# Kernel optimization log

Hardware: AMD Instinct MI355X
Metric: run time of the kernel (lower is better)

Reference implementation:

```python
import jax, jax.numpy as jnp
import numpy as np

N_EMBEDS = 1024
N_HEADS = 16
EPS = 1e-3


def layer_norm(x, gamma, beta):
    mean = jnp.mean(x, axis=-1, keepdims=True)
    var = jnp.mean((x - mean) ** 2, axis=-1, keepdims=True)
    return gamma * (x - mean) / jnp.sqrt(var + EPS) + beta


def setup_inputs() -> dict:
    key = jax.random.key(0)
    ks = jax.random.split(key, 8)
    B, T, C = 4, 2048, N_EMBEDS
    s = 1.0 / np.sqrt(C)
    return {
        "x": jax.random.normal(ks[0], (B, T, C), dtype=jnp.float32),
        "w_qkv": jax.random.normal(ks[1], (C, 3 * C), dtype=jnp.float32) * s,
        "w_proj": jax.random.normal(ks[2], (C, C), dtype=jnp.float32) * s,
        "b_proj": jnp.zeros((C,), dtype=jnp.float32),
        "w1": jax.random.normal(ks[3], (C, 4 * C), dtype=jnp.float32) * s,
        "b1": jnp.zeros((4 * C,), dtype=jnp.float32),
        "w2": jax.random.normal(ks[4], (4 * C, C), dtype=jnp.float32) * (0.5 / np.sqrt(C)),
        "b2": jnp.zeros((C,), dtype=jnp.float32),
        "gamma1": jnp.ones((C,), dtype=jnp.float32),
        "beta1": jnp.zeros((C,), dtype=jnp.float32),
        "gamma2": jnp.ones((C,), dtype=jnp.float32),
        "beta2": jnp.zeros((C,), dtype=jnp.float32),
    }


def reference(x, w_qkv, w_proj, b_proj, w1, b1, w2, b2, gamma1, beta1, gamma2, beta2):
    B, T, C = x.shape
    H = N_HEADS
    D = C // H
    scale = D ** -0.5

    # --- attention sub-layer (pre-LN) ---
    h = layer_norm(x, gamma1, beta1)
    qkv = h @ w_qkv                      # [B,T,3C]
    q, k, v = jnp.split(qkv, 3, axis=-1)
    q = q.reshape(B, T, H, D).transpose(0, 2, 1, 3)  # [B,H,T,D]
    k = k.reshape(B, T, H, D).transpose(0, 2, 1, 3)
    v = v.reshape(B, T, H, D).transpose(0, 2, 1, 3)
    att = jnp.einsum('bhqd,bhkd->bhqk', q, k) * scale
    causal = jnp.tril(jnp.ones((T, T), dtype=bool))
    att = jnp.where(causal[None, None], att, jnp.float32(-1e9))
    att = jax.nn.softmax(att, axis=-1)
    out = jnp.einsum('bhqk,bhkd->bhqd', att, v)
    out = out.transpose(0, 2, 1, 3).reshape(B, T, C)
    x = x + out @ w_proj + b_proj

    # --- FFN sub-layer (pre-LN, erf-GELU) ---
    h = layer_norm(x, gamma2, beta2)
    h = jax.nn.gelu(h @ w1 + b1, approximate=False)
    x = x + h @ w2 + b2
    return x
```

## Files before the change

### kernel.cpp

```cpp
#include <hip/hip_runtime.h>
#include <hip/hip_bf16.h>
#include <cstdint>
#include <cstddef>

#define B_ 4
#define T_ 2048
#define C_ 1024
#define H_ 16
#define D_ 64
#define M_ (B_*T_)

using bf16_t = __hip_bfloat16;
typedef __bf16 v8bf __attribute__((ext_vector_type(8)));
typedef float  v4f  __attribute__((ext_vector_type(4)));
typedef float  f32x16 __attribute__((ext_vector_type(16)));

#define QSCALE (0.125f * 1.44269504088896340736f)

static __device__ __forceinline__ bf16_t f2bf(float v){ return __float2bfloat16(v); }
static __device__ __forceinline__ float bfraw2f(unsigned short u){
  union { unsigned int i; float f; } c; c.i = ((unsigned int)u) << 16; return c.f;
}

static __device__ __forceinline__ void glds16(const bf16_t* g, bf16_t* l){
  __builtin_amdgcn_global_load_lds((__attribute__((address_space(1))) void*)g,
                                   (__attribute__((address_space(3))) void*)l, 16, 0, 0);
}

static __device__ __forceinline__ uint32_t cvt_pk_bf16(float lo, float hi){
  uint32_t w;
  asm("v_cvt_pk_bf16_f32 %0, %1, %2" : "=v"(w) : "v"(lo), "v"(hi));
  return w;
}

static __device__ __forceinline__ float gelu_fast(float x){
  const float u = __builtin_fmaf(0.044715f * x * x, x, x);
  const float e = __builtin_amdgcn_exp2f(2.3021256637f * u);
  return x - x * __builtin_amdgcn_rcpf(1.0f + e);
}

__global__ void k_transpose_all(const float* __restrict__ in0, bf16_t* __restrict__ out0,
                                const float* __restrict__ in1, bf16_t* __restrict__ out1,
                                const float* __restrict__ in2, bf16_t* __restrict__ out2,
                                const float* __restrict__ in3, bf16_t* __restrict__ out3){
  __shared__ float tile[32][33];
  const int bid = blockIdx.x;
  const float* in; bf16_t* out; int K, N, lb;
  if (bid < 3072)      { in=in0; out=out0; K=1024; N=3072; lb=bid; }
  else if (bid < 4096) { in=in1; out=out1; K=1024; N=1024; lb=bid-3072; }
  else if (bid < 8192) { in=in2; out=out2; K=1024; N=4096; lb=bid-4096; }
  else                 { in=in3; out=out3; K=4096; N=1024; lb=bid-8192; }
  const int nbx = N >> 5;
  const int k0 = (lb / nbx) * 32, n0 = (lb % nbx) * 32;
  const int tx = threadIdx.x, ty = threadIdx.y;
  #pragma unroll
  for(int j=0;j<32;j+=8) tile[ty+j][tx] = in[(size_t)(k0+ty+j)*N + n0+tx];
  __syncthreads();
  #pragma unroll
  for(int j=0;j<32;j+=8) out[(size_t)(n0+ty+j)*K + k0+tx] = f2bf(tile[tx][ty+j]);
}

__global__ __launch_bounds__(256) void k_layernorm(const float* __restrict__ x,
                                                   const float* __restrict__ gamma,
                                                   const float* __restrict__ beta,
                                                   bf16_t* __restrict__ out){
  int row = blockIdx.x;
  int tid = threadIdx.x;
  const float4 v = reinterpret_cast<const float4*>(x + (size_t)row*C_)[tid];
  float s  = v.x+v.y+v.z+v.w;
  float ss = v.x*v.x+v.y*v.y+v.z*v.z+v.w*v.w;
  #pragma unroll
  for(int m=1;m<64;m<<=1){ s += __shfl_xor(s,m); ss += __shfl_xor(ss,m); }
  __shared__ float sbuf[4], ssbuf[4];
  int wid = tid>>6, lane = tid&63;
  if(lane==0){ sbuf[wid]=s; ssbuf[wid]=ss; }
  __syncthreads();
  s  = sbuf[0]+sbuf[1]+sbuf[2]+sbuf[3];
  ss = ssbuf[0]+ssbuf[1]+ssbuf[2]+ssbuf[3];
  float mean = s * (1.0f/C_);
  float var  = ss * (1.0f/C_) - mean*mean;
  float rstd = rsqrtf(var + 1e-3f);
  const float4 g = reinterpret_cast<const float4*>(gamma)[tid];
  const float4 b = reinterpret_cast<const float4*>(beta)[tid];
  union { ushort4 u; bf16_t h[4]; } pk;
  pk.h[0] = f2bf(g.x*(v.x-mean)*rstd + b.x);
  pk.h[1] = f2bf(g.y*(v.y-mean)*rstd + b.y);
  pk.h[2] = f2bf(g.z*(v.z-mean)*rstd + b.z);
  pk.h[3] = f2bf(g.w*(v.w-mean)*rstd + b.w);
  *reinterpret_cast<ushort4*>(out + (size_t)row*C_ + tid*4) = pk.u;
}

__global__ __launch_bounds__(256)
void k_add2(const bf16_t* __restrict__ p0, const bf16_t* __restrict__ p1,
            const float* __restrict__ bias, float* out){
  const int row = blockIdx.x, tid = threadIdx.x;
  float4 xr = reinterpret_cast<const float4*>(out + (size_t)row*C_)[tid];
  const ushort4 a = reinterpret_cast<const ushort4*>(p0 + (size_t)row*C_)[tid];
  const ushort4 b = reinterpret_cast<const ushort4*>(p1 + (size_t)row*C_)[tid];
  const float4 g = reinterpret_cast<const float4*>(bias)[tid];
  xr.x += bfraw2f(a.x) + bfraw2f(b.x) + g.x;
  xr.y += bfraw2f(a.y) + bfraw2f(b.y) + g.y;
  xr.z += bfraw2f(a.z) + bfraw2f(b.z) + g.z;
  xr.w += bfraw2f(a.w) + bfraw2f(b.w) + g.w;
  reinterpret_cast<float4*>(out + (size_t)row*C_)[tid] = xr;
}

template<int MODE>
__global__ __launch_bounds__(512, 1)
void k_gemm9(const bf16_t* __restrict__ A, const bf16_t* __restrict__ Bt,
             const float* __restrict__ bias, const float* resid,
             void* out0, void* out1, void* out2,
             int N, int ld, int klen, int gx, int tc)
{
  __shared__ __align__(16) bf16_t As[2][2][128*64];
  __shared__ __align__(16) bf16_t Bs[2][2][128*64];
  const int tid = threadIdx.x, lane = tid & 63, w = tid >> 6;
  const int wm = w >> 2, wn = w & 3;
  const int koff = blockIdx.z * klen;

  const int sswz = ((lane & 7) ^ ((lane >> 3) & 7)) * 8;
  const int srow = w * 8 + (lane >> 3);

  int row0, col0;
  const bf16_t *Agb, *Bgb;
  auto set_tile = [&](int tile){
    const int swz = (tile & 7) * (tc >> 3) + (tile >> 3);
    const int ct = swz % gx, rt = swz / gx;
    row0 = rt * 256; col0 = ct * 256;
    Agb = A  + (size_t)(row0 + srow) * ld + koff + sswz;
    Bgb = Bt + (size_t)(col0 + srow) * ld + koff + sswz;
  };

  auto stageA = [&](int tt, int hh){
    const bf16_t* src = Agb + (size_t)(hh * 128) * ld + tt * 64;
    bf16_t* dst = &As[tt & 1][hh][w * 512];
    glds16(src, dst);
    glds16(src + (size_t)64 * ld, dst + 4096);
  };
  auto stageB = [&](int tt, int hh){
    const bf16_t* src = Bgb + (size_t)(hh * 128) * ld + tt * 64;
    bf16_t* dst = &Bs[tt & 1][hh][w * 512];
    glds16(src, dst);
    glds16(src + (size_t)64 * ld, dst + 4096);
  };
  auto stage_prologue = [&](){
    stageA(0,0); stageA(0,1); stageB(0,0); stageB(0,1);
    stageB(1,0); stageB(1,1); stageA(1,0);
  };

  v8bf af[4][2], bfv[4][2];
  v4f acc[8][4];

  auto LDA = [&](int bb, int mh){
    const bf16_t* base = &As[bb][wm][0];
    #pragma unroll
    for (int m = 0; m < 4; ++m)
      #pragma unroll
      for (int kk = 0; kk < 2; ++kk) {
        const int r  = mh*64 + m*16 + (lane & 15);
        const int sl = (kk*4 + (lane >> 4)) ^ (lane & 7);
        af[m][kk] = *reinterpret_cast<const v8bf*>(base + r*64 + sl*8);
      }
  };
  auto LDB4 = [&](int bb, int nh){
    const bf16_t* base = &Bs[bb][wn >> 1][0];
    #pragma unroll
    for (int n = 0; n < 2; ++n)
      #pragma unroll
      for (int kk = 0; kk < 2; ++kk) {
        const int r  = (wn & 1)*64 + (nh*2+n)*16 + (lane & 15);
        const int sl = (kk*4 + (lane >> 4)) ^ (lane & 7);
        bfv[nh*2+n][kk] = *reinterpret_cast<const v8bf*>(base + r*64 + sl*8);
      }
  };

#define MFMA_Q(mh_, nh_) \
  __builtin_amdgcn_s_setprio(1); \
  _Pragma("unroll") \
  for (int kk = 0; kk < 2; ++kk) \
    _Pragma("unroll") \
    for (int m = 0; m < 4; ++m) \
      _Pragma("unroll") \
      for (int n = 0; n < 2; ++n) \
        acc[(mh_)*4+m][(nh_)*2+n] = __builtin_amdgcn_mfma_f32_16x16x32_bf16( \
            af[m][kk], bfv[(nh_)*2+n][kk], acc[(mh_)*4+m][(nh_)*2+n], 0,0,0); \
  __builtin_amdgcn_s_setprio(0);

#define BAR()   __builtin_amdgcn_s_barrier()
#define LGKM0() do { asm volatile("s_waitcnt lgkmcnt(0)" ::: "memory"); \
                     __builtin_amdgcn_sched_barrier(0); } while(0)

  const int NP = (klen >> 6) >> 1;
  int tile = blockIdx.x;
  set_tile(tile);
  stage_prologue();

  for (;;) {
    asm volatile("s_waitcnt vmcnt(6)" ::: "memory");
    BAR();
    #pragma unroll
    for (int mf = 0; mf < 8; ++mf)
      #pragma unroll
      for (int nf = 0; nf < 4; ++nf)
        acc[mf][nf] = (v4f){0.f, 0.f, 0.f, 0.f};

    for (int j = 0; j < NP; ++j) {
      const int t2 = 2*j + 2, t3 = 2*j + 3;
      const bool more = (j + 1 < NP);
      LDA(0, 0); LDB4(0, 0);
      stageA(2*j + 1, 1);
      BAR(); LGKM0(); MFMA_Q(0, 0); BAR();
      LDB4(0, 1);
      if (more) stageB(t2, 0);
      BAR(); LGKM0(); MFMA_Q(0, 1); BAR();
      LDA(0, 1);
      if (more) stageB(t2, 1);
      BAR(); LGKM0(); MFMA_Q(1, 0); BAR();
      if (more) { stageA(t2, 0); asm volatile("s_waitcnt vmcnt(6)" ::: "memory"); }
      else      {                asm volatile("s_waitcnt vmcnt(0)" ::: "memory"); }
      BAR(); MFMA_Q(1, 1); BAR();
      LDA(1, 0); LDB4(1, 0);
      if (more) stageA(t2, 1);
      BAR(); LGKM0(); MFMA_Q(0, 0); BAR();
      LDB4(1, 1);
      if (more) stageB(t3, 0);
      BAR(); LGKM0(); MFMA_Q(0, 1); BAR();
      LDA(1, 1);
      if (more) stageB(t3, 1);
      BAR(); LGKM0(); MFMA_Q(1, 0); BAR();
      if (more) { stageA(t3, 0); asm volatile("s_waitcnt vmcnt(6)" ::: "memory"); }
      else      {                asm volatile("s_waitcnt vmcnt(0)" ::: "memory"); }
      BAR(); MFMA_Q(1, 1); BAR();
    }

    const int erow0 = row0, ecol0 = col0;
    const int next = tile + (int)gridDim.x;
    const bool have_next = (next < tc);
    if (have_next) { set_tile(next); stage_prologue(); }

    #pragma unroll
    for (int mf = 0; mf < 8; ++mf) {
      const int rbase = erow0 + wm*128 + mf*16 + (lane>>4)*4;
      #pragma unroll
      for (int nf = 0; nf < 4; ++nf) {
        const int c = ecol0 + wn*64 + nf*16 + (lane&15);
        #pragma unroll
        for (int i = 0; i < 4; ++i) {
          const int rr = rbase + i;
          float v = acc[mf][nf][i];
          if constexpr(MODE==0){
            const int sec = c >> 10, cc = c & 1023;
            const int h = cc >> 6, d = cc & 63;
            const int b = rr >> 11, t = rr & 2047;
            if(sec==0)      ((bf16_t*)out0)[((size_t)(b*H_ + h)*T_ + t)*D_ + d] = f2bf(v * QSCALE);
            else if(sec==1) ((bf16_t*)out1)[((size_t)(b*H_ + h)*T_ + t)*D_ + d] = f2bf(v);
            else            ((bf16_t*)out2)[((size_t)(b*H_ + h)*D_ + d)*T_ + t] = f2bf(v);
          } else if constexpr(MODE==2){
            ((bf16_t*)out0)[(size_t)rr*N + c] = f2bf(gelu_fast(v + bias[c]));
          } else {
            bf16_t* dst = blockIdx.z ? (bf16_t*)out1 : (bf16_t*)out0;
            dst[(size_t)rr*N + c] = f2bf(v);
          }
        }
      }
    }
    if (!have_next) break;
    tile = next;
  }
#undef MFMA_Q
#undef BAR
#undef LGKM0
}

__global__ __launch_bounds__(512, 1)
void k_gemm8(const bf16_t* __restrict__ A, const bf16_t* __restrict__ Bt,
             const float* __restrict__ bias, const float* resid,
             float* out0, int N, int K, int gx)
{
  __shared__ __align__(16) bf16_t As[2][256*64];
  __shared__ __align__(16) bf16_t Bs[3][128*64];
  const int tid = threadIdx.x, lane = tid & 63, w = tid >> 6;
  const int wm = w >> 1, wn = w & 1;

  const int nwg = gx * 32;
  const int orig = blockIdx.y * gx + blockIdx.x;
  const int swz = (orig & 7) * (nwg >> 3) + (orig >> 3);
  const int ct = swz % gx, rt = swz / gx;
  const int row0 = rt * 256, col0 = ct * 128;

  const int sswz = ((lane & 7) ^ ((lane >> 3) & 7)) * 8;
  const int srow = w * 8 + (lane >> 3);
  const bf16_t* Agb = A  + (size_t)(row0 + srow) * K + sswz;
  const bf16_t* Bgb = Bt + (size_t)(col0 + srow) * K + sswz;

  auto stageA = [&](int tt){
    const bf16_t* src = Agb + tt * 64;
    bf16_t* dst = &As[tt & 1][w * 512];
    #pragma unroll
    for (int i = 0; i < 4; ++i)
      glds16(src + (size_t)(i*64) * K, dst + i*4096);
  };
  auto stageB = [&](int tt){
    const bf16_t* src = Bgb + tt * 64;
    bf16_t* dst = &Bs[tt % 3][w * 512];
    #pragma unroll
    for (int i = 0; i < 2; ++i)
      glds16(src + (size_t)(i*64) * K, dst + i*4096);
  };

  v8bf af[4][2], bfv[4][2];
  v4f acc[4][4] = {};

  auto LDA = [&](int ab){
    const bf16_t* base = &As[ab][0];
    #pragma unroll
    for (int m = 0; m < 4; ++m)
      #pragma unroll
      for (int kk = 0; kk < 2; ++kk) {
        const int r  = wm*64 + m*16 + (lane & 15);
        const int sl = (kk*4 + (lane >> 4)) ^ (lane & 7);
        af[m][kk] = *reinterpret_cast<const v8bf*>(base + r*64 + sl*8);
      }
  };
  auto LDB = [&](int bb, int nh){
    const bf16_t* base = &Bs[bb][0];
    #pragma unroll
    for (int n = 0; n < 2; ++n)
      #pragma unroll
      for (int kk = 0; kk < 2; ++kk) {
        const int r  = wn*64 + (nh*2+n)*16 + (lane & 15);
        const int sl = (kk*4 + (lane >> 4)) ^ (lane & 7);
        bfv[nh*2+n][kk] = *reinterpret_cast<const v8bf*>(base + r*64 + sl*8);
      }
  };

#define MFMA_Q(nh_) \
  __builtin_amdgcn_s_setprio(1); \
  _Pragma("unroll") \
  for (int kk = 0; kk < 2; ++kk) \
    _Pragma("unroll") \
    for (int m = 0; m < 4; ++m) \
      _Pragma("unroll") \
      for (int n = 0; n < 2; ++n) \
        acc[m][(nh_)*2+n] = __builtin_amdgcn_mfma_f32_16x16x32_bf16( \
            af[m][kk], bfv[(nh_)*2+n][kk], acc[m][(nh_)*2+n], 0,0,0); \
  __builtin_amdgcn_s_setprio(0);

#define BAR()   __builtin_amdgcn_s_barrier()
#define LGKM0() do { asm volatile("s_waitcnt lgkmcnt(0)" ::: "memory"); \
                     __builtin_amdgcn_sched_barrier(0); } while(0)
#define VM6()   asm volatile("s_waitcnt vmcnt(6)" ::: "memory")
#define VM0()   asm volatile("s_waitcnt vmcnt(0)" ::: "memory")

  const int NP = (K >> 6) >> 1;
  stageB(0); stageA(0); stageB(1); stageA(1);
  VM6();
  BAR();

  for (int j = 0; j < NP; ++j) {
    const int t0 = 2*j, t1 = 2*j + 1, t2 = 2*j + 2, t3 = 2*j + 3;
    const bool more = (j + 1 < NP);
    LDA(0); LDB(t0 % 3, 0);
    if (more) stageB(t2);
    BAR(); LGKM0(); MFMA_Q(0); BAR();
    LDB(t0 % 3, 1);
    if (more) { stageA(t2); VM6(); } else { VM0(); }
    BAR(); LGKM0(); MFMA_Q(1); BAR();
    LDA(1); LDB(t1 % 3, 0);
    if (more) stageB(t3);
    BAR(); LGKM0(); MFMA_Q(0); BAR();
    LDB(t1 % 3, 1);
    if (more) { stageA(t3); VM6(); } else { VM0(); }
    BAR(); LGKM0(); MFMA_Q(1); BAR();
  }
#undef MFMA_Q
#undef BAR
#undef LGKM0
#undef VM6
#undef VM0

  #pragma unroll
  for (int mf = 0; mf < 4; ++mf) {
    const int rbase = row0 + wm*64 + mf*16 + (lane>>4)*4;
    #pragma unroll
    for (int nf = 0; nf < 4; ++nf) {
      const int c = col0 + wn*64 + nf*16 + (lane&15);
      #pragma unroll
      for (int i = 0; i < 4; ++i) {
        const int rr = rbase + i;
        out0[(size_t)rr*N + c] = acc[mf][nf][i] + bias[c] + resid[(size_t)rr*N + c];
      }
    }
  }
}

__global__ __launch_bounds__(256)
void k_attn(const bf16_t* __restrict__ Q, const bf16_t* __restrict__ Kg,
            const bf16_t* __restrict__ Vt, bf16_t* __restrict__ O)
{
  __shared__ __align__(16) bf16_t Ks [64][72];
  __shared__ __align__(16) bf16_t Vts[64][72];
  __shared__ __align__(16) bf16_t Os [128][72];
  const int bh = blockIdx.y;
  const int pair = blockIdx.x;
  const int tid = threadIdx.x, lane = tid & 63, w = tid >> 6;
  const int ql = lane & 31, hi = lane >> 5;
  const int srow = tid >> 2;
  const int scol = (tid & 3) * 16;
  const bf16_t* Kgp = Kg + ((size_t)bh*T_ + srow)*D_ + scol;
  const bf16_t* Vtp = Vt + ((size_t)bh*D_ + srow)*T_ + scol;
  const int b = bh >> 4, h = bh & 15;

  for(int half=0; half<2; ++half){
    const int qt = half ? pair : (15 - pair);
    const int qbase = qt*128 + w*32;
    const int q = qbase + ql;

    v8bf qf[4];
    {
      const bf16_t* Qb = Q + ((size_t)bh*T_ + q)*D_ + hi*8;
      #pragma unroll
      for(int ds=0; ds<4; ds++)
        qf[ds] = *reinterpret_cast<const v8bf*>(Qb + ds*16);
    }

    f32x16 accO[2] = {};
    float mrun = -1e30f, lrun = 0.0f;
    const int NT = (qt + 1) * 2;

    v8bf kr0 = *reinterpret_cast<const v8bf*>(Kgp);
    v8bf kr1 = *reinterpret_cast<const v8bf*>(Kgp + 8);
    v8bf vr0 = *reinterpret_cast<const v8bf*>(Vtp);
    v8bf vr1 = *reinterpret_cast<const v8bf*>(Vtp + 8);

    for(int t=0; t<NT; t++){
      const int kv0 = t*64;
      *reinterpret_cast<v8bf*>(&Ks [srow][scol  ]) = kr0;
      *reinterpret_cast<v8bf*>(&Ks [srow][scol+8]) = kr1;
      *reinterpret_cast<v8bf*>(&Vts[srow][scol  ]) = vr0;
      *reinterpret_cast<v8bf*>(&Vts[srow][scol+8]) = vr1;
      __syncthreads();
      if(t+1 < NT){
        const size_t kn = (size_t)(kv0 + 64);
        kr0 = *reinterpret_cast<const v8bf*>(Kgp + kn*D_);
        kr1 = *reinterpret_cast<const v8bf*>(Kgp + kn*D_ + 8);
        vr0 = *reinterpret_cast<const v8bf*>(Vtp + kn);
        vr1 = *reinterpret_cast<const v8bf*>(Vtp + kn + 8);
      }

      if(kv0 <= qbase + 31){
        f32x16 sT[2] = {};
        #pragma unroll
        for(int kvh=0; kvh<2; kvh++)
          #pragma unroll
          for(int ds=0; ds<4; ds++){
            v8bf kf = *reinterpret_cast<const v8bf*>(&Ks[kvh*32 + ql][ds*16 + hi*8]);
            sT[kvh] = __builtin_amdgcn_mfma_f32_32x32x16_bf16(kf, qf[ds], sT[kvh], 0,0,0);
          }

        if(kv0 + 63 > qbase){
          const int qrel = q - kv0 - hi*4;
          #pragma unroll
          for(int kvh=0; kvh<2; kvh++)
            #pragma unroll
            for(int r=0; r<16; r++){
              const int c = kvh*32 + (r&3) + 8*(r>>2);
              if(c > qrel) sT[kvh][r] = -1e30f;
            }
        }

        float pm = sT[0][0];
        #pragma unroll
        for(int r=1; r<16; r++) pm = fmaxf(pm, sT[0][r]);
        #pragma unroll
        for(int r=0; r<16; r++) pm = fmaxf(pm, sT[1][r]);
        pm = fmaxf(pm, __shfl_xor(pm, 32));

        if(__any(pm - mrun > 8.0f)){
          const float mnew = fmaxf(mrun, pm);
          const float corr = __builtin_amdgcn_exp2f(mrun - mnew);
          mrun = mnew;
          lrun *= corr;
          #pragma unroll
          for(int dh=0; dh<2; dh++)
            #pragma unroll
            for(int r=0; r<16; r++) accO[dh][r] *= corr;
        }

        float rs = 0.0f;
        #pragma unroll
        for(int kvh=0; kvh<2; kvh++)
          #pragma unroll
          for(int r=0; r<16; r++){
            float p = __builtin_amdgcn_exp2f(sT[kvh][r] - mrun);
            sT[kvh][r] = p;
            rs += p;
          }
        rs += __shfl_xor(rs, 32);
        lrun += rs;

        v8bf pfrag[4];
        #pragma unroll
        for(int s4=0; s4<4; s4++){
          const int kvh = s4>>1, bb = (s4&1)*8;
          uint32_t wa = cvt_pk_bf16(sT[kvh][bb+0], sT[kvh][bb+1]);
          uint32_t wb = cvt_pk_bf16(sT[kvh][bb+2], sT[kvh][bb+3]);
          uint32_t wc = cvt_pk_bf16(sT[kvh][bb+4], sT[kvh][bb+5]);
          uint32_t wd = cvt_pk_bf16(sT[kvh][bb+6], sT[kvh][bb+7]);
          uint32_t xwa = (uint32_t)__shfl_xor((int)wa, 32);
          uint32_t xwb = (uint32_t)__shfl_xor((int)wb, 32);
          uint32_t xwc = (uint32_t)__shfl_xor((int)wc, 32);
          uint32_t xwd = (uint32_t)__shfl_xor((int)wd, 32);
          union { uint32_t u[4]; v8bf v; } pk;
          pk.u[0] = hi ? xwc : wa;
          pk.u[1] = hi ? xwd : wb;
          pk.u[2] = hi ? wc  : xwa;
          pk.u[3] = hi ? wd  : xwb;
          pfrag[s4] = pk.v;
        }

        #pragma unroll
        for(int dh=0; dh<2; dh++)
          #pragma unroll
          for(int s4=0; s4<4; s4++){
            v8bf vf = *reinterpret_cast<const v8bf*>(&Vts[dh*32 + ql][s4*16 + hi*8]);
            accO[dh] = __builtin_amdgcn_mfma_f32_32x32x16_bf16(vf, pfrag[s4], accO[dh], 0,0,0);
          }
      }
      __syncthreads();
    }

    const float inv = 1.0f / lrun;
    #pragma unroll
    for(int dh=0; dh<2; dh++)
      #pragma unroll
      for(int rg=0; rg<4; rg++){
        uint32_t lo_ = cvt_pk_bf16(accO[dh][rg*4+0]*inv, accO[dh][rg*4+1]*inv);
        uint32_t hi_ = cvt_pk_bf16(accO[dh][rg*4+2]*inv, accO[dh][rg*4+3]*inv);
        uint2 w2; w2.x = lo_; w2.y = hi_;
        *reinterpret_cast<uint2*>(&Os[w*32 + ql][dh*32 + rg*8 + hi*4]) = w2;
      }
    __syncthreads();
    const int orow = tid >> 1, ocol = (tid & 1) * 32;
    bf16_t* Og = O + ((size_t)(b*T_ + qt*128 + orow))*C_ + h*64 + ocol;
    #pragma unroll
    for(int j=0;j<4;j++)
      *reinterpret_cast<v8bf*>(Og + j*8) = *reinterpret_cast<const v8bf*>(&Os[orow][ocol + j*8]);
    __syncthreads();
  }
}

extern "C" void kernel_launch(void* const* d_in, const int* in_sizes, int n_in,
                              void* d_out, int out_size, void* d_ws, size_t ws_size,
                              hipStream_t stream) {
  const float* x      = (const float*)d_in[0];
  const float* w_qkv  = (const float*)d_in[1];
  const float* w_proj = (const float*)d_in[2];
  const float* b_proj = (const float*)d_in[3];
  const float* w1     = (const float*)d_in[4];
  const float* b1     = (const float*)d_in[5];
  const float* w2     = (const float*)d_in[6];
  const float* b2     = (const float*)d_in[7];
  const float* gamma1 = (const float*)d_in[8];
  const float* beta1  = (const float*)d_in[9];
  const float* gamma2 = (const float*)d_in[10];
  const float* beta2  = (const float*)d_in[11];

  char* ws = (char*)d_ws;
  bf16_t* wqkv_t  = (bf16_t*)(ws + 0);
  bf16_t* wproj_t = (bf16_t*)(ws + 6291456);
  bf16_t* w1_t    = (bf16_t*)(ws + 8388608);
  bf16_t* w2_t    = (bf16_t*)(ws + 16777216);
  bf16_t* qb      = (bf16_t*)(ws + 25165824);
  bf16_t* kb      = (bf16_t*)(ws + 41943040);
  bf16_t* vtb     = (bf16_t*)(ws + 58720256);
  bf16_t* obuf    = (bf16_t*)(ws + 75497472);
  bf16_t* hb      = (bf16_t*)(ws + 92274688);
  bf16_t* gb      = (bf16_t*)(ws + 25165824);
  float*  x2      = (float*)d_out;

  k_transpose_all<<<12288, dim3(32,8), 0, stream>>>(w_qkv, wqkv_t, w_proj, wproj_t,
                                                    w1, w1_t, w2, w2_t);

  k_layernorm<<<M_, 256, 0, stream>>>(x, gamma1, beta1, hb);

  k_gemm9<0><<<dim3(256, 1, 1), 512, 0, stream>>>(hb, wqkv_t, nullptr, nullptr,
                                                  qb, kb, vtb, 3072, 1024, 1024, 12, 384);
  k_attn<<<dim3(8, B_*H_), 256, 0, stream>>>(qb, kb, vtb, obuf);

  k_gemm8<<<dim3(8, 32), 512, 0, stream>>>(obuf, wproj_t, b_proj, x,
                                           x2, 1024, 1024, 8);
  k_layernorm<<<M_, 256, 0, stream>>>(x2, gamma2, beta2, hb);

  k_gemm9<2><<<dim3(256, 1, 1), 512, 0, stream>>>(hb, w1_t, b1, nullptr,
                                                  gb, nullptr, nullptr, 4096, 1024, 1024, 16, 512);
  k_gemm9<4><<<dim3(128, 1, 2), 512, 0, stream>>>(gb, w2_t, nullptr, nullptr,
                                                  obuf, hb, nullptr, 1024, 4096, 2048, 4, 128);
  k_add2<<<M_, 256, 0, stream>>>(obuf, hb, b2, x2);
}
```

Before: 369.4 us.

## Add 128x128-tile persistent GEMM kernel with 2 blocks/CU for FFN up-projection

Introduces k_gemmH, a persistent bf16 MFMA GEMM using 128x128 output tiles, 256-thread blocks and a two-stage K-pipelined LDS schedule with launch bounds allowing two workgroups per CU. It replaces the larger-tile 512-thread k_gemm9<2> for the FFN first matmul with GELU epilogue. The intent is better occupancy and latency hiding through smaller tiles and more concurrent workgroups. The cost is lower per-tile data reuse and more global traffic for A and B.

```diff
diff --git a/kernel.cpp b/kernel.cpp
--- a/kernel.cpp
+++ b/kernel.cpp
@@ -272,6 +272,157 @@
 #undef LGKM0
 }
 
+__global__ __launch_bounds__(256, 2)
+void k_gemmH(const bf16_t* __restrict__ A, const bf16_t* __restrict__ Bt,
+             const float* __restrict__ bias, bf16_t* __restrict__ out0,
+             int N, int ld, int klen, int gx, int tc)
+{
+  __shared__ __align__(16) bf16_t As[2][2][64*64];
+  __shared__ __align__(16) bf16_t Bs[2][2][64*64];
+  const int tid = threadIdx.x, lane = tid & 63, w = tid >> 6;
+  const int wm = w >> 1, wn = w & 1;
+
+  const int sswz = ((lane & 7) ^ ((lane >> 3) & 7)) * 8;
+  const int srow = w * 8 + (lane >> 3);
+
+  int row0, col0;
+  const bf16_t *Agb, *Bgb;
+  auto set_tile = [&](int tile){
+    const int swz = (tile & 7) * (tc >> 3) + (tile >> 3);
+    const int ct = swz % gx, rt = swz / gx;
+    row0 = rt * 128; col0 = ct * 128;
+    Agb = A  + (size_t)(row0 + srow) * ld + sswz;
+    Bgb = Bt + (size_t)(col0 + srow) * ld + sswz;
+  };
+
+  auto stageA = [&](int tt, int hh){
+    const bf16_t* src = Agb + (size_t)(hh * 64) * ld + tt * 64;
+    bf16_t* dst0 = &As[tt & 1][hh][w * 512];
+    glds16(src, dst0);
+    glds16(src + (size_t)32 * ld, dst0 + 2048);
+  };
+  auto stageB = [&](int tt, int hh){
+    const bf16_t* src = Bgb + (size_t)(hh * 64) * ld + tt * 64;
+    bf16_t* dst0 = &Bs[tt & 1][hh][w * 512];
+    glds16(src, dst0);
+    glds16(src + (size_t)32 * ld, dst0 + 2048);
+  };
+  auto stage_prologue = [&](){
+    stageA(0,0); stageA(0,1); stageB(0,0); stageB(0,1);
+    stageB(1,0); stageB(1,1); stageA(1,0);
+  };
+
+  v8bf af[2][2], bfv[4][2];
+  v4f acc[4][4];
+
+  auto LDA = [&](int bb, int mh){
+    const bf16_t* base = &As[bb][wm][0];
+    #pragma unroll
+    for (int m = 0; m < 2; ++m)
+      #pragma unroll
+      for (int kk = 0; kk < 2; ++kk) {
+        const int r  = mh*32 + m*16 + (lane & 15);
+        const int sl = (kk*4 + (lane >> 4)) ^ (lane & 7);
+        af[m][kk] = *reinterpret_cast<const v8bf*>(base + r*64 + sl*8);
+      }
+  };
+  auto LDB4 = [&](int bb, int nh){
+    const bf16_t* base = &Bs[bb][wn][0];
+    #pragma unroll
+    for (int n = 0; n < 2; ++n)
+      #pragma unroll
+      for (int kk = 0; kk < 2; ++kk) {
+        const int r  = (nh*2+n)*16 + (lane & 15);
+        const int sl = (kk*4 + (lane >> 4)) ^ (lane & 7);
+        bfv[nh*2+n][kk] = *reinterpret_cast<const v8bf*>(base + r*64 + sl*8);
+      }
+  };
+
+#define MFMA_Q(mh_, nh_) \
+  __builtin_amdgcn_s_setprio(1); \
+  _Pragma("unroll") \
+  for (int kk = 0; kk < 2; ++kk) \
+    _Pragma("unroll") \
+    for (int m = 0; m < 2; ++m) \
+      _Pragma("unroll") \
+      for (int n = 0; n < 2; ++n) \
+        acc[(mh_)*2+m][(nh_)*2+n] = __builtin_amdgcn_mfma_f32_16x16x32_bf16( \
+            af[m][kk], bfv[(nh_)*2+n][kk], acc[(mh_)*2+m][(nh_)*2+n], 0,0,0); \
+  __builtin_amdgcn_s_setprio(0);
+
+#define BAR()   __builtin_amdgcn_s_barrier()
+#define LGKM0() do { asm volatile("s_waitcnt lgkmcnt(0)" ::: "memory"); \
+                     __builtin_amdgcn_sched_barrier(0); } while(0)
+
+  const int NP = (klen >> 6) >> 1;
+  int tile = blockIdx.x;
+  set_tile(tile);
+  stage_prologue();
+
+  for (;;) {
+    asm volatile("s_waitcnt vmcnt(6)" ::: "memory");
+    BAR();
+    #pragma unroll
+    for (int mf = 0; mf < 4; ++mf)
+      #pragma unroll
+      for (int nf = 0; nf < 4; ++nf)
+        acc[mf][nf] = (v4f){0.f, 0.f, 0.f, 0.f};
+
+    for (int j = 0; j < NP; ++j) {
+      const int t2 = 2*j + 2, t3 = 2*j + 3;
+      const bool more = (j + 1 < NP);
+      LDA(0, 0); LDB4(0, 0);
+      stageA(2*j + 1, 1);
+      BAR(); LGKM0(); MFMA_Q(0, 0); BAR();
+      LDB4(0, 1);
+      if (more) stageB(t2, 0);
+      BAR(); LGKM0(); MFMA_Q(0, 1); BAR();
+      LDA(0, 1);
+      if (more) stageB(t2, 1);
+      BAR(); LGKM0(); MFMA_Q(1, 0); BAR();
+      if (more) { stageA(t2, 0); asm volatile("s_waitcnt vmcnt(6)" ::: "memory"); }
+      else      {                asm volatile("s_waitcnt vmcnt(0)" ::: "memory"); }
+      BAR(); MFMA_Q(1, 1); BAR();
+      LDA(1, 0); LDB4(1, 0);
+      if (more) stageA(t2, 1);
+      BAR(); LGKM0(); MFMA_Q(0, 0); BAR();
+      LDB4(1, 1);
+      if (more) stageB(t3, 0);
+      BAR(); LGKM0(); MFMA_Q(0, 1); BAR();
+      LDA(1, 1);
+      if (more) stageB(t3, 1);
+      BAR(); LGKM0(); MFMA_Q(1, 0); BAR();
+      if (more) { stageA(t3, 0); asm volatile("s_waitcnt vmcnt(6)" ::: "memory"); }
+      else      {                asm volatile("s_waitcnt vmcnt(0)" ::: "memory"); }
+      BAR(); MFMA_Q(1, 1); BAR();
+    }
+
+    const int erow0 = row0, ecol0 = col0;
+    const int next = tile + (int)gridDim.x;
+    const bool have_next = (next < tc);
+    if (have_next) { set_tile(next); stage_prologue(); }
+
+    #pragma unroll
+    for (int mf = 0; mf < 4; ++mf) {
+      const int rbase = erow0 + wm*64 + mf*16 + (lane>>4)*4;
+      #pragma unroll
+      for (int nf = 0; nf < 4; ++nf) {
+        const int c = ecol0 + wn*64 + nf*16 + (lane&15);
+        #pragma unroll
+        for (int i = 0; i < 4; ++i) {
+          const int rr = rbase + i;
+          out0[(size_t)rr*N + c] = f2bf(gelu_fast(acc[mf][nf][i] + bias[c]));
+        }
+      }
+    }
+    if (!have_next) break;
+    tile = next;
+  }
+#undef MFMA_Q
+#undef BAR
+#undef LGKM0
+}
+
 __global__ __launch_bounds__(512, 1)
 void k_gemm8(const bf16_t* __restrict__ A, const bf16_t* __restrict__ Bt,
              const float* __restrict__ bias, const float* resid,
@@ -592,8 +743,8 @@
                                            x2, 1024, 1024, 8);
   k_layernorm<<<M_, 256, 0, stream>>>(x2, gamma2, beta2, hb);
 
-  k_gemm9<2><<<dim3(256, 1, 1), 512, 0, stream>>>(hb, w1_t, b1, nullptr,
-                                                  gb, nullptr, nullptr, 4096, 1024, 1024, 16, 512);
+  k_gemmH<<<dim3(512, 1, 1), 256, 0, stream>>>(hb, w1_t, b1, gb,
+                                               4096, 1024, 1024, 32, 2048);
   k_gemm9<4><<<dim3(128, 1, 2), 512, 0, stream>>>(gb, w2_t, nullptr, nullptr,
                                                   obuf, hb, nullptr, 1024, 4096, 2048, 4, 128);
   k_add2<<<M_, 256, 0, stream>>>(obuf, hb, b2, x2);
```

Result: slower. 380.4 us (+3.0%).

## Restructure GEMM main loop into two half-phases with full A-fragment loads

Applied to the files above, without the earlier changes.

Loads all eight A fragments per K-tile at once and runs 8x2 MFMA blocks per phase, so each K-tile takes two barrier-delimited phases instead of four. The B and A global-to-LDS stage issues are regrouped to match. This halves the number of barriers and LDS wait points per K-tile, aiming to cut synchronization overhead. In exchange it holds twice as many A-fragment registers, which raises VGPR pressure, and it bunches the global loads into fewer, larger bursts.

```diff
diff --git a/kernel.cpp b/kernel.cpp
--- a/kernel.cpp
+++ b/kernel.cpp
@@ -148,19 +148,21 @@
     stageB(1,0); stageB(1,1); stageA(1,0);
   };
 
-  v8bf af[4][2], bfv[4][2];
+  v8bf af[8][2], bfv[4][2];
   v4f acc[8][4];
 
-  auto LDA = [&](int bb, int mh){
+  auto LDA16 = [&](int bb){
     const bf16_t* base = &As[bb][wm][0];
     #pragma unroll
-    for (int m = 0; m < 4; ++m)
-      #pragma unroll
-      for (int kk = 0; kk < 2; ++kk) {
-        const int r  = mh*64 + m*16 + (lane & 15);
-        const int sl = (kk*4 + (lane >> 4)) ^ (lane & 7);
-        af[m][kk] = *reinterpret_cast<const v8bf*>(base + r*64 + sl*8);
-      }
+    for (int mh = 0; mh < 2; ++mh)
+      #pragma unroll
+      for (int m = 0; m < 4; ++m)
+        #pragma unroll
+        for (int kk = 0; kk < 2; ++kk) {
+          const int r  = mh*64 + m*16 + (lane & 15);
+          const int sl = (kk*4 + (lane >> 4)) ^ (lane & 7);
+          af[mh*4+m][kk] = *reinterpret_cast<const v8bf*>(base + r*64 + sl*8);
+        }
   };
   auto LDB4 = [&](int bb, int nh){
     const bf16_t* base = &Bs[bb][wn >> 1][0];
@@ -174,16 +176,16 @@
       }
   };
 
-#define MFMA_Q(mh_, nh_) \
+#define MFMA_Q2(nh_) \
   __builtin_amdgcn_s_setprio(1); \
   _Pragma("unroll") \
   for (int kk = 0; kk < 2; ++kk) \
     _Pragma("unroll") \
-    for (int m = 0; m < 4; ++m) \
+    for (int mf = 0; mf < 8; ++mf) \
       _Pragma("unroll") \
       for (int n = 0; n < 2; ++n) \
-        acc[(mh_)*4+m][(nh_)*2+n] = __builtin_amdgcn_mfma_f32_16x16x32_bf16( \
-            af[m][kk], bfv[(nh_)*2+n][kk], acc[(mh_)*4+m][(nh_)*2+n], 0,0,0); \
+        acc[mf][(nh_)*2+n] = __builtin_amdgcn_mfma_f32_16x16x32_bf16( \
+            af[mf][kk], bfv[(nh_)*2+n][kk], acc[mf][(nh_)*2+n], 0,0,0); \
   __builtin_amdgcn_s_setprio(0);
 
 #define BAR()   __builtin_amdgcn_s_barrier()
@@ -207,30 +209,22 @@
     for (int j = 0; j < NP; ++j) {
       const int t2 = 2*j + 2, t3 = 2*j + 3;
       const bool more = (j + 1 < NP);
-      LDA(0, 0); LDB4(0, 0);
+      LDA16(0); LDB4(0, 0);
       stageA(2*j + 1, 1);
-      BAR(); LGKM0(); MFMA_Q(0, 0); BAR();
+      BAR(); LGKM0(); MFMA_Q2(0); BAR();
       LDB4(0, 1);
-      if (more) stageB(t2, 0);
-      BAR(); LGKM0(); MFMA_Q(0, 1); BAR();
-      LDA(0, 1);
-      if (more) stageB(t2, 1);
-      BAR(); LGKM0(); MFMA_Q(1, 0); BAR();
-      if (more) { stageA(t2, 0); asm volatile("s_waitcnt vmcnt(6)" ::: "memory"); }
-      else      {                asm volatile("s_waitcnt vmcnt(0)" ::: "memory"); }
-      BAR(); MFMA_Q(1, 1); BAR();
-      LDA(1, 0); LDB4(1, 0);
+      if (more) { stageB(t2, 0); stageB(t2, 1); stageA(t2, 0);
+                  asm volatile("s_waitcnt vmcnt(6)" ::: "memory"); }
+      else      { asm volatile("s_waitcnt vmcnt(0)" ::: "memory"); }
+      BAR(); LGKM0(); MFMA_Q2(1); BAR();
+      LDA16(1); LDB4(1, 0);
       if (more) stageA(t2, 1);
-      BAR(); LGKM0(); MFMA_Q(0, 0); BAR();
+      BAR(); LGKM0(); MFMA_Q2(0); BAR();
       LDB4(1, 1);
-      if (more) stageB(t3, 0);
-      BAR(); LGKM0(); MFMA_Q(0, 1); BAR();
-      LDA(1, 1);
-      if (more) stageB(t3, 1);
-      BAR(); LGKM0(); MFMA_Q(1, 0); BAR();
-      if (more) { stageA(t3, 0); asm volatile("s_waitcnt vmcnt(6)" ::: "memory"); }
-      else      {                asm volatile("s_waitcnt vmcnt(0)" ::: "memory"); }
-      BAR(); MFMA_Q(1, 1); BAR();
+      if (more) { stageB(t3, 0); stageB(t3, 1); stageA(t3, 0);
+                  asm volatile("s_waitcnt vmcnt(6)" ::: "memory"); }
+      else      { asm volatile("s_waitcnt vmcnt(0)" ::: "memory"); }
+      BAR(); LGKM0(); MFMA_Q2(1); BAR();
     }
 
     const int erow0 = row0, ecol0 = col0;
@@ -267,7 +261,7 @@
     if (!have_next) break;
     tile = next;
   }
-#undef MFMA_Q
+#undef MFMA_Q2
 #undef BAR
 #undef LGKM0
 }
```

After: 445.2 us. +20.5%, slower.
